# Optimization experiments

Measured on AMD Instinct MI355X. Metric: run time of the kernel, lower is better.

The kernel has to match this reference:

```python
import jax, jax.numpy as jnp
from jax import lax
import numpy as np

B, H0, W0, C = 2, 192, 192, 192
CH = C // 2            # channels per attention branch (window / stripe)
D = 4                  # blocks in the stage
WS = 8                 # window / stripe size
NHW = 4                # window-attention heads
NHS = 4                # stripe-attention heads
ADF = 2                # anchor down factor (avgpool)
MLP_RATIO = 4

def _rel_pos_index(ws):
    coords = np.stack(np.meshgrid(np.arange(ws), np.arange(ws), indexing="ij"))
    coords = coords.reshape(2, -1)
    rel = coords[:, :, None] - coords[:, None, :]
    rel = rel.transpose(1, 2, 0) + (ws - 1)
    return rel[..., 0] * (2 * ws - 1) + rel[..., 1]

REL_IDX = jnp.asarray(_rel_pos_index(WS))  # [N, N] into (2*WS-1)^2 table

def _swin_mask(H, W, ws, shift):
    img = np.zeros((H, W))
    cnt = 0
    for hs in (slice(0, -ws), slice(-ws, -shift), slice(-shift, None)):
        for wsl in (slice(0, -ws), slice(-ws, -shift), slice(-shift, None)):
            img[hs, wsl] = cnt
            cnt += 1
    win = img.reshape(H // ws, ws, W // ws, ws).transpose(0, 2, 1, 3).reshape(-1, ws * ws)
    diff = win[:, None, :] - win[:, :, None]
    return jnp.asarray(np.where(diff != 0, -100.0, 0.0), jnp.float32)

def _ln(x, g, b):
    mu = x.mean(-1, keepdims=True)
    var = x.var(-1, keepdims=True)
    return (x - mu) * lax.rsqrt(var + 1e-5) * g + b

def _window_attn(xw, H, W, shift, qkv_w, qkv_b, rpb):
    Bb, L, Cw = xw.shape
    h, dh, N = NHW, Cw // NHW, WS * WS
    x = xw.reshape(Bb, H, W, Cw)
    if shift:
        x = jnp.roll(x, (-shift, -shift), (1, 2))
    nH, nW = H // WS, W // WS
    xw_ = x.reshape(Bb, nH, WS, nW, WS, Cw).transpose(0, 1, 3, 2, 4, 5).reshape(-1, N, Cw)
    qkv = (xw_ @ qkv_w + qkv_b).reshape(-1, N, 3, h, dh)
    q, k, v = qkv[:, :, 0], qkv[:, :, 1], qkv[:, :, 2]
    attn = jnp.einsum("wnhd,wmhd->whnm", q * dh ** -0.5, k)
    attn = attn + rpb[REL_IDX].transpose(2, 0, 1)[None]  # relative position bias [h,N,N]
    if shift:
        mask = _swin_mask(H, W, WS, shift)  # [nWin, N, N]
        attn = (attn.reshape(Bb, nH * nW, h, N, N) + mask[None, :, None]).reshape(-1, h, N, N)
    attn = jax.nn.softmax(attn, -1)
    out = jnp.einsum("whnm,wmhd->wnhd", attn, v).reshape(-1, N, Cw)
    x = out.reshape(Bb, nH, nW, WS, WS, Cw).transpose(0, 1, 3, 2, 4, 5).reshape(Bb, H, W, Cw)
    if shift:
        x = jnp.roll(x, (shift, shift), (1, 2))
    return x.reshape(Bb, L, Cw)

def _stripe_attn(xs, H, W, qkv_w, qkv_b):
    # anchored stripe attention: q -> anchors -> k/v (two small softmaxes)
    Bb, L, Cs = xs.shape
    h, dh, N = NHS, Cs // NHS, WS * WS
    M = (WS // ADF) * (WS // ADF)
    x = xs.reshape(Bb, H // WS, WS, W // WS, WS, Cs).transpose(0, 1, 3, 2, 4, 5)
    x = x.reshape(-1, WS, WS, Cs)
    anchor = x.reshape(-1, WS // ADF, ADF, WS // ADF, ADF, Cs).mean((2, 4)).reshape(-1, M, h, dh)
    xt = x.reshape(-1, N, Cs)
    qkv = (xt @ qkv_w + qkv_b).reshape(-1, N, 3, h, dh)
    q, k, v = qkv[:, :, 0], qkv[:, :, 1], qkv[:, :, 2]
    s = dh ** -0.5
    a1 = jax.nn.softmax(jnp.einsum("snhd,smhd->shnm", q * s, anchor), -1)  # [S,h,N,M]
    a2 = jax.nn.softmax(jnp.einsum("smhd,snhd->shmn", anchor * s, k), -1)  # [S,h,M,N]
    out = jnp.einsum("shnm,shmt,sthd->snhd", a1, a2, v).reshape(-1, N, Cs)
    out = out.reshape(Bb, H // WS, W // WS, WS, WS, Cs).transpose(0, 1, 3, 2, 4, 5)
    return out.reshape(Bb, L, Cs)

def setup_inputs() -> dict:
    key = jax.random.key(0)
    ks = jax.random.split(key, 8)
    std = 0.02
    return {
        "x": jax.random.normal(ks[0], (B, H0 * W0, C), jnp.float32),
        "norm1_g": jnp.ones((D, C), jnp.float32),
        "norm1_b": jnp.zeros((D, C), jnp.float32),
        "qkv_w_win": jax.random.normal(ks[1], (D, CH, 3 * CH), jnp.float32) * std,
        "qkv_b_win": jnp.zeros((D, 3 * CH), jnp.float32),
        "qkv_w_str": jax.random.normal(ks[2], (D, CH, 3 * CH), jnp.float32) * std,
        "qkv_b_str": jnp.zeros((D, 3 * CH), jnp.float32),
        "proj_w": jax.random.normal(ks[3], (D, C, C), jnp.float32) * std,
        "proj_b": jnp.zeros((D, C), jnp.float32),
        "rpb_table": jax.random.normal(ks[4], (D, (2 * WS - 1) ** 2, NHW), jnp.float32) * std,
        "norm2_g": jnp.ones((D, C), jnp.float32),
        "norm2_b": jnp.zeros((D, C), jnp.float32),
        "fc1_w": jax.random.normal(ks[5], (D, C, MLP_RATIO * C), jnp.float32) * std,
        "fc1_b": jnp.zeros((D, MLP_RATIO * C), jnp.float32),
        "fc2_w": jax.random.normal(ks[6], (D, MLP_RATIO * C, C), jnp.float32) * std,
        "fc2_b": jnp.zeros((D, C), jnp.float32),
        "conv_w": jax.random.normal(ks[7], (C, C, 3, 3), jnp.float32) * std,
        "conv_b": jnp.zeros((C,), jnp.float32),
        "H": H0,
        "W": W0,
    }

def reference(x, norm1_g, norm1_b, qkv_w_win, qkv_b_win, qkv_w_str, qkv_b_str,
              proj_w, proj_b, rpb_table, norm2_g, norm2_b, fc1_w, fc1_b,
              fc2_w, fc2_b, conv_w, conv_b, H, W):
    res0 = x
    for i in range(D):
        xn = _ln(x, norm1_g[i], norm1_b[i])
        shift = WS // 2 if i % 2 == 0 else 0  # window_shift = i % 2 == 0
        ow = _window_attn(xn[..., :CH], H, W, shift, qkv_w_win[i], qkv_b_win[i], rpb_table[i])
        os_ = _stripe_attn(xn[..., CH:], H, W, qkv_w_str[i], qkv_b_str[i])
        x = x + (jnp.concatenate([ow, os_], -1) @ proj_w[i] + proj_b[i])
        xn2 = _ln(x, norm2_g[i], norm2_b[i])
        x = x + (jax.nn.gelu(xn2 @ fc1_w[i] + fc1_b[i]) @ fc2_w[i] + fc2_b[i])
    Bb = x.shape[0]
    xc = x.reshape(Bb, H, W, C).transpose(0, 3, 1, 2)
    y = lax.conv_general_dilated(xc, conv_w, (1, 1), "SAME") + conv_b[None, :, None, None]
    y = y.transpose(0, 2, 3, 1).reshape(Bb, H * W, C)
    return y + res0  # long residual of the TransformerStage
```

## Files before the change

### kernel.cpp

```cpp
#include <hip/hip_runtime.h>
#include <math.h>

typedef __bf16 bf16_t;
typedef bf16_t bf16x8 __attribute__((ext_vector_type(8)));
typedef bf16_t bf16x4 __attribute__((ext_vector_type(4)));
typedef float f32x4 __attribute__((ext_vector_type(4)));

#define TOKS 73728
#define CCH 192

__device__ __forceinline__ float gelu_f(float x) {
  float x2 = x*x;
  float u = 1.5957691216057308f * x * fmaf(0.044715f, x2, 1.0f);
  float e = __expf(-u);
  return x * __builtin_amdgcn_rcpf(1.0f + e);
}

__device__ __forceinline__ void glds16(const void* g, void* l) {
  __builtin_amdgcn_global_load_lds(
      (const __attribute__((address_space(1))) void*)g,
      (__attribute__((address_space(3))) void*)l, 16, 0, 0);
}

__global__ void prep_all_k(const float* __restrict__ qw, const float* __restrict__ qs,
// ... 208 lines not shown
      for (int mi=0;mi<4;++mi)
        #pragma unroll
        for (int ni=0;ni<3;++ni)
          acc[mi][ni] = __builtin_amdgcn_mfma_f32_16x16x32_bf16(af[mi], bfr[ni], acc[mi][ni], 0, 0, 0);
    }
    __syncthreads();
  }

  #pragma unroll
  for (int mi=0;mi<4;++mi) {
    #pragma unroll
    for (int ni=0;ni<3;++ni) {
      const int col = wn*48 + ni*16 + lr;
      const float bs = bias[col];
      #pragma unroll
      for (int e=0;e<4;++e) {
        const long row = m0 + wm*64 + mi*16 + lk*4 + e;
        float v = acc[mi][ni][e] + bs + resid[row*CCH + col];
        acc[mi][ni][e] = v;
        resid[row*CCH + col] = v;
        if (EPI == 1) xnout[row*CCH + col] = (bf16_t)v;
      }
    }
  }
  if (EPI == 0) {
    float* red  = (float*)&As[0][0];
    float* stat = red + 1024;
    #pragma unroll
    for (int mi=0;mi<4;++mi) {
      #pragma unroll
      for (int e=0;e<4;++e) {
        float p1 = acc[mi][0][e] + acc[mi][1][e] + acc[mi][2][e];
        float p2 = acc[mi][0][e]*acc[mi][0][e] + acc[mi][1][e]*acc[mi][1][e]
                 + acc[mi][2][e]*acc[mi][2][e];
        #pragma unroll
        for (int off=1; off<16; off<<=1) {
          p1 += __shfl_xor(p1, off);
          p2 += __shfl_xor(p2, off);
        }
        if (lr == 0) {
          const int r = wm*64 + mi*16 + lk*4 + e;
          red[(r*4 + wn)*2]     = p1;
          red[(r*4 + wn)*2 + 1] = p2;
        }
      }
    }
    __syncthreads();
    if (tid < 128) {
      const int r = tid;
      float s1 = red[(r*4+0)*2] + red[(r*4+1)*2] + red[(r*4+2)*2] + red[(r*4+3)*2];
      float s2 = red[(r*4+0)*2+1] + red[(r*4+1)*2+1] + red[(r*4+2)*2+1] + red[(r*4+3)*2+1];
      const float mu = s1 * (1.f/CCH);
      stat[r*2]   = mu;
      stat[r*2+1] = rsqrtf(s2*(1.f/CCH) - mu*mu + 1e-5f);
    }
    __syncthreads();
    #pragma unroll
    for (int mi=0;mi<4;++mi) {
      #pragma unroll
      for (int e=0;e<4;++e) {
        const int r = wm*64 + mi*16 + lk*4 + e;
        const float mu = stat[r*2], rstd = stat[r*2+1];
        #pragma unroll
        for (int ni=0;ni<3;++ni) {
          const int col = wn*48 + ni*16 + lr;
          xnout[(m0+r)*CCH + col] = (bf16_t)((acc[mi][ni][e]-mu)*rstd*gg[col] + bb[col]);
        }
      }
    }
  }
}

__global__ __launch_bounds__(512) void gemmf_k(
    const bf16_t* __restrict__ A,
    const bf16_t* __restrict__ Bt,
    const float* __restrict__ bias,
    bf16_t* __restrict__ outb) {
  constexpr int BK=64, MASK=7;
  __shared__ bf16_t As[2][128*64];
  __shared__ bf16_t Bs[2][192*64];
  const int tid = threadIdx.x;
  const int w = tid >> 6, l = tid & 63;
  const int lr = l & 15, lk = l >> 4;
  const int ri = l >> 3, si = l & 7;
  const int wm = w >> 2, wn = w & 3;
  const long m0 = (long)blockIdx.x * 128;
  const int n0 = blockIdx.y * 192;

  f32x4 acc[4][3];
  #pragma unroll
  for (int mi=0;mi<4;++mi)
    #pragma unroll
    for (int ni=0;ni<3;++ni) acc[mi][ni] = (f32x4){0.f,0.f,0.f,0.f};

  auto stage = [&](int buf, int k0) {
    #pragma unroll
    for (int j = 0; j < 2; ++j) {
      const int s = j*8 + w;
      const int gr = s*8 + ri;
      glds16(A + (m0+gr)*192L + k0 + ((si ^ (gr&MASK))*8), &As[buf][s*512]);
    }
    #pragma unroll
    for (int j = 0; j < 3; ++j) {
      const int s = j*8 + w;
      const int gr = s*8 + ri;
      glds16(Bt + (long)(n0+gr)*192 + k0 + ((si ^ (gr&MASK))*8), &Bs[buf][s*512]);
    }
  };

  stage(0, 0);
  __syncthreads();
  for (int kt = 0; kt < 3; ++kt) {
    const int cur = kt & 1;
    if (kt + 1 < 3) stage(cur^1, (kt+1)*BK);
    #pragma unroll
    for (int ks = 0; ks < 2; ++ks) {
      bf16x8 af[4], bfr[3];
      #pragma unroll
      for (int mi=0;mi<4;++mi) {
        const int ar = wm*64 + mi*16 + lr;
        const int slot = (ks*4 + lk) ^ (ar & MASK);
        af[mi] = *(const bf16x8*)(&As[cur][ar*64 + slot*8]);
      }
      #pragma unroll
      for (int ni=0;ni<3;++ni) {
        const int br = wn*48 + ni*16 + lr;
        const int slot = (ks*4 + lk) ^ (br & MASK);
        bfr[ni] = *(const bf16x8*)(&Bs[cur][br*64 + slot*8]);
      }
      #pragma unroll
      for (int mi=0;mi<4;++mi)
        #pragma unroll
        for (int ni=0;ni<3;++ni)
          acc[mi][ni] = __builtin_amdgcn_mfma_f32_16x16x32_bf16(af[mi], bfr[ni], acc[mi][ni], 0, 0, 0);
    }
    __syncthreads();
  }

  #pragma unroll
  for (int mi=0;mi<4;++mi) {
    #pragma unroll
    for (int ni=0;ni<3;++ni) {
      const int col = n0 + wn*48 + ni*16 + lr;
      const float bs = bias[col];
      #pragma unroll
      for (int e=0;e<4;++e) {
        const long row = m0 + wm*64 + mi*16 + lk*4 + e;
        outb[row*768 + col] = (bf16_t)gelu_f(acc[mi][ni][e] + bs);
      }
    }
  }
}

__global__ __launch_bounds__(256) void win_attn3_k(
    const bf16_t* __restrict__ qkv, bf16_t* __restrict__ aout,
    const float* __restrict__ rpb2, int shift) {
  __shared__ bf16_t Vs[4][64][28];
  __shared__ bf16_t Pl[4][64][68];
  __shared__ float invl[4][64];
  const int h = threadIdx.x >> 6, l = threadIdx.x & 63;
  const int c = l & 15, g = l >> 4;
  const int wblk = blockIdx.x;
  const int b = wblk / 576, wi = wblk % 576;
  const int wh = wi / 24, ww = wi % 24;

  auto gtok = [&](int t) -> long {
    int ho = wh*8 + (t>>3) + shift; if (ho >= 192) ho -= 192;
    int wo = ww*8 + (t&7) + shift;  if (wo >= 192) wo -= 192;
    return (long)b*36864 + (long)ho*192 + wo;
  };

  {
    const bf16_t* vsrc = qkv + gtok(l)*576 + 192 + h*24;
    #pragma unroll
    for (int j=0;j<3;++j) {
      bf16x4 lo = *(const bf16x4*)(vsrc + j*8);
      bf16x4 hi = *(const bf16x4*)(vsrc + j*8 + 4);
      *(bf16x4*)(&Vs[h][l][j*8])   = lo;
      *(bf16x4*)(&Vs[h][l][j*8+4]) = hi;
    }
    *(bf16x4*)(&Vs[h][l][24]) = (bf16x4){};
  }

  bf16x8 kf[4], qf[4];
  #pragma unroll
  for (int t=0;t<4;++t) {
    bf16x8 z = {};
    kf[t] = z; qf[t] = z;
    if (g < 3) {
      const bf16_t* pb = qkv + gtok(16*t + c)*576 + h*24 + g*8;
      qf[t] = *(const bf16x8*)(pb);
      kf[t] = *(const bf16x8*)(pb + 96);
    }
  }

  f32x4 st[4][4];
  #pragma unroll
  for (int mt=0;mt<4;++mt)
    #pragma unroll
    for (int nt=0;nt<4;++nt)
      st[mt][nt] = __builtin_amdgcn_mfma_f32_16x16x32_bf16(kf[mt], qf[nt], (f32x4){0.f,0.f,0.f,0.f}, 0, 0, 0);

  const float scale = 0.20412414523193154f;
  const float4* rp = (const float4*)rpb2 + (h*64*16 + c);
  #pragma unroll
  for (int mt=0;mt<4;++mt) {
    #pragma unroll
    for (int r=0;r<4;++r) {
      const int k = 16*mt + 4*g + r;
      float4 b4 = rp[k*16];
      st[mt][0][r] = fmaf(st[mt][0][r], scale, b4.x);
      st[mt][1][r] = fmaf(st[mt][1][r], scale, b4.y);
      st[mt][2][r] = fmaf(st[mt][2][r], scale, b4.z);
      st[mt][3][r] = fmaf(st[mt][3][r], scale, b4.w);
    }
  }

  if (shift && (wh==23 || ww==23)) {
    #pragma unroll
    for (int mt=0;mt<4;++mt)
      #pragma unroll
      for (int r=0;r<4;++r) {
        const int kk = 16*mt + 4*g + r;
        const int krc = (wh==23) ? (((kk>>3)<4)?1:2) : 0;
        const int kcc = (ww==23) ? (((kk&7)<4)?1:2) : 0;
        const int kcls = krc*3 + kcc;
        #pragma unroll
        for (int nt=0;nt<4;++nt) {
          const int qq = 16*nt + c;
          const int qrc = (wh==23) ? (((qq>>3)<4)?1:2) : 0;
          const int qcc = (ww==23) ? (((qq&7)<4)?1:2) : 0;
          if (qrc*3 + qcc != kcls) st[mt][nt][r] -= 100.f;
        }
      }
  }

  #pragma unroll
  for (int nt=0;nt<4;++nt) {
    float m = st[0][nt][0];
    #pragma unroll
    for (int mt=0;mt<4;++mt)
      #pragma unroll
      for (int r=0;r<4;++r) m = fmaxf(m, st[mt][nt][r]);
    m = fmaxf(m, __shfl_xor(m, 16));
    m = fmaxf(m, __shfl_xor(m, 32));
    float s = 0.f;
    #pragma unroll
    for (int mt=0;mt<4;++mt)
      #pragma unroll
      for (int r=0;r<4;++r) {
        float p = __expf(st[mt][nt][r] - m);
        st[mt][nt][r] = p;
        s += p;
      }
    s += __shfl_xor(s, 16);
    s += __shfl_xor(s, 32);
    if (g == 0) invl[h][16*nt + c] = 1.f / s;
  }

  #pragma unroll
  for (int mt=0;mt<4;++mt) {
    #pragma unroll
    for (int nt=0;nt<4;++nt) {
      const int q = 16*nt + c;
      const int sl = (4*mt + g) ^ ((q&7)<<1);
      bf16x4 pk;
      #pragma unroll
      for (int r=0;r<4;++r) pk[r] = (bf16_t)st[mt][nt][r];
      *(bf16x4*)(&Pl[h][q][sl*4]) = pk;
    }
  }

  f32x4 oa[4][2];
  #pragma unroll
  for (int mt=0;mt<4;++mt)
    #pragma unroll
    for (int nt=0;nt<2;++nt) oa[mt][nt] = (f32x4){0.f,0.f,0.f,0.f};

  #pragma unroll
  for (int s2=0;s2<2;++s2) {
    bf16x8 pfr[4];
    #pragma unroll
    for (int mt=0;mt<4;++mt) {
      const int q = 16*mt + c;
      const int S0 = (8*s2 + 2*g) ^ ((q&7)<<1);
      bf16x4 lo = *(const bf16x4*)(&Pl[h][q][S0*4]);
      bf16x4 hi = *(const bf16x4*)(&Pl[h][q][S0*4 + 4]);
      #pragma unroll
      for (int r=0;r<4;++r) { pfr[mt][r] = lo[r]; pfr[mt][4+r] = hi[r]; }
    }
    #pragma unroll
    for (int nt=0;nt<2;++nt) {
      const int d = 16*nt + c;
      const int deff = (d < 24) ? d : 24;
      bf16x8 vf;
      #pragma unroll
      for (int e=0;e<8;++e) vf[e] = Vs[h][32*s2 + 8*g + e][deff];
      #pragma unroll
      for (int mt=0;mt<4;++mt)
        oa[mt][nt] = __builtin_amdgcn_mfma_f32_16x16x32_bf16(pfr[mt], vf, oa[mt][nt], 0, 0, 0);
    }
  }

  #pragma unroll
  for (int mt=0;mt<4;++mt) {
    #pragma unroll
    for (int r=0;r<4;++r) {
      const int q = 16*mt + 4*g + r;
      const float inv = invl[h][q];
      bf16_t* ob = aout + gtok(q)*192 + h*24;
      #pragma unroll
      for (int nt=0;nt<2;++nt) {
        const int d = 16*nt + c;
        if (d < 24) ob[d] = (bf16_t)(oa[mt][nt][r] * inv);
      }
    }
  }
}

__global__ __launch_bounds__(256) void stripe_attn3_k(
    const bf16_t* __restrict__ qkv, const bf16_t* __restrict__ xn,
    bf16_t* __restrict__ aout) {
  __shared__ bf16_t Vs[4][64][28];
  __shared__ bf16_t Ans[4][16][40];
  __shared__ bf16_t a2s[4][16][68];
  __shared__ bf16_t a1s[4][64][24];
  __shared__ bf16_t Ts2[4][32][28];
  const int h = threadIdx.x >> 6, l = threadIdx.x & 63;
  const int c = l & 15, g = l >> 4;
  const int wblk = blockIdx.x;
  const int b = wblk / 576, wi = wblk % 576;
  const int wh = wi / 24, ww = wi % 24;
  const long base0 = (long)b*36864 + (long)(wh*8)*192 + ww*8;
  auto gtok = [&](int t) -> long { return base0 + (long)(t>>3)*192 + (t&7); };

  {
    const bf16_t* vsrc = qkv + gtok(l)*576 + 480 + h*24;
    #pragma unroll
    for (int j=0;j<3;++j) {
      *(bf16x4*)(&Vs[h][l][j*8])   = *(const bf16x4*)(vsrc + j*8);
      *(bf16x4*)(&Vs[h][l][j*8+4]) = *(const bf16x4*)(vsrc + j*8 + 4);
    }
    *(bf16x4*)(&Vs[h][l][24]) = (bf16x4){};
  }
  {
    const int m = l >> 2, dq = l & 3;
    const int ar = m >> 2, ac = m & 3;
    const bf16_t* t0 = xn + (base0 + (long)(2*ar)*192 + 2*ac)*192 + 96 + h*24;
    #pragma unroll
    for (int j=0;j<6;++j) {
      const int d = dq*6 + j;
      float ssum = (float)t0[d] + (float)t0[192+d] + (float)t0[36864+d] + (float)t0[37056+d];
      Ans[h][m][d] = (bf16_t)(0.25f*ssum);
    }
  }
  if (l < 16) {
    *(bf16x4*)(&Ans[h][l][24]) = (bf16x4){};
    *(bf16x4*)(&Ans[h][l][28]) = (bf16x4){};
    bf16_t* z = &Ts2[h][16+l][0];
    #pragma unroll
    for (int j=0;j<7;++j) *(bf16x4*)(z + j*4) = (bf16x4){};
    *(bf16x4*)(&Ts2[h][l][24]) = (bf16x4){};
  }

  bf16x8 anf = *(const bf16x8*)(&Ans[h][c][g*8]);

  bf16x8 kf[4], qf[4];
  #pragma unroll
  for (int t=0;t<4;++t) {
    const bf16_t* pb = qkv + gtok(16*t + c)*576 + 288 + h*24 + g*8;
    qf[t] = *(const bf16x8*)(pb);
    kf[t] = *(const bf16x8*)(pb + 96);
  }

  const float scale = 0.20412414523193154f;

  f32x4 st2[4];
  #pragma unroll
  for (int mt=0;mt<4;++mt)
    st2[mt] = __builtin_amdgcn_mfma_f32_16x16x32_bf16(kf[mt], anf, (f32x4){0.f,0.f,0.f,0.f}, 0, 0, 0);

  {
    float m2 = -1e30f;
    #pragma unroll
    for (int mt=0;mt<4;++mt)
      #pragma unroll
      for (int r=0;r<4;++r) { st2[mt][r] *= scale; m2 = fmaxf(m2, st2[mt][r]); }
    m2 = fmaxf(m2, __shfl_xor(m2, 16));
    m2 = fmaxf(m2, __shfl_xor(m2, 32));
    float s = 0.f;
    #pragma unroll
    for (int mt=0;mt<4;++mt)
      #pragma unroll
      for (int r=0;r<4;++r) { float p = __expf(st2[mt][r] - m2); st2[mt][r] = p; s += p; }
    s += __shfl_xor(s, 16);
    s += __shfl_xor(s, 32);
    const float inv = 1.f / s;
    #pragma unroll
    for (int mt=0;mt<4;++mt) {
      const int sl = (4*mt + g) ^ ((c&7)<<1);
      bf16x4 pk;
      #pragma unroll
      for (int r=0;r<4;++r) pk[r] = (bf16_t)(st2[mt][r] * inv);
      *(bf16x4*)(&a2s[h][c][sl*4]) = pk;
    }
  }

  f32x4 ta[2];
  ta[0] = (f32x4){0.f,0.f,0.f,0.f}; ta[1] = (f32x4){0.f,0.f,0.f,0.f};
  #pragma unroll
  for (int kt=0;kt<2;++kt) {
    const int S0 = (8*kt + 2*g) ^ ((c&7)<<1);
    bf16x4 lo = *(const bf16x4*)(&a2s[h][c][S0*4]);
    bf16x4 hi = *(const bf16x4*)(&a2s[h][c][S0*4 + 4]);
    bf16x8 pf;
    #pragma unroll
    for (int r=0;r<4;++r) { pf[r] = lo[r]; pf[4+r] = hi[r]; }
    #pragma unroll
    for (int nt2=0;nt2<2;++nt2) {
      const int d = 16*nt2 + c;
      const int deff = (d < 24) ? d : 24;
      bf16x8 vf;
      #pragma unroll
      for (int e=0;e<8;++e) vf[e] = Vs[h][kt*32 + 8*g + e][deff];
      ta[nt2] = __builtin_amdgcn_mfma_f32_16x16x32_bf16(pf, vf, ta[nt2], 0, 0, 0);
    }
  }
  #pragma unroll
  for (int nt2=0;nt2<2;++nt2) {
    const int d = 16*nt2 + c;
    if (d < 24) {
      #pragma unroll
      for (int r=0;r<4;++r) Ts2[h][4*g + r][d] = (bf16_t)ta[nt2][r];
    }
  }

  f32x4 st1[4];
  #pragma unroll
  for (int nt=0;nt<4;++nt)
    st1[nt] = __builtin_amdgcn_mfma_f32_16x16x32_bf16(anf, qf[nt], (f32x4){0.f,0.f,0.f,0.f}, 0, 0, 0);

  #pragma unroll
  for (int nt=0;nt<4;++nt) {
    float m1 = -1e30f;
    #pragma unroll
    for (int r=0;r<4;++r) { st1[nt][r] *= scale; m1 = fmaxf(m1, st1[nt][r]); }
    m1 = fmaxf(m1, __shfl_xor(m1, 16));
    m1 = fmaxf(m1, __shfl_xor(m1, 32));
    float s = 0.f;
    #pragma unroll
    for (int r=0;r<4;++r) { float p = __expf(st1[nt][r] - m1); st1[nt][r] = p; s += p; }
    s += __shfl_xor(s, 16);
    s += __shfl_xor(s, 32);
    const float inv1 = 1.f / s;
    bf16x4 ak;
    #pragma unroll
    for (int r=0;r<4;++r) ak[r] = (bf16_t)(st1[nt][r] * inv1);
    *(bf16x4*)(&a1s[h][16*nt + c][4*g]) = ak;
  }

  f32x4 oa[4][2];
  #pragma unroll
  for (int mt=0;mt<4;++mt) { oa[mt][0] = (f32x4){0.f,0.f,0.f,0.f}; oa[mt][1] = (f32x4){0.f,0.f,0.f,0.f}; }
  #pragma unroll
  for (int mt=0;mt<4;++mt) {
    bf16x8 af = {};
    if (g < 2) af = *(const bf16x8*)(&a1s[h][16*mt + c][g*8]);
    #pragma unroll
    for (int nt2=0;nt2<2;++nt2) {
      const int d = 16*nt2 + c;
      const int deff = (d < 24) ? d : 24;
      bf16x8 tf;
      #pragma unroll
      for (int e=0;e<8;++e) tf[e] = Ts2[h][8*g + e][deff];
      oa[mt][nt2] = __builtin_amdgcn_mfma_f32_16x16x32_bf16(af, tf, oa[mt][nt2], 0, 0, 0);
    }
  }

  #pragma unroll
  for (int mt=0;mt<4;++mt) {
    #pragma unroll
    for (int r=0;r<4;++r) {
      const int tw = 16*mt + 4*g + r;
      bf16_t* ob = aout + gtok(tw)*192 + 96 + h*24;
      #pragma unroll
      for (int nt2=0;nt2<2;++nt2) {
        const int d = 16*nt2 + c;
        if (d < 24) ob[d] = (bf16_t)(oa[mt][nt2][r]);
      }
    }
  }
}

__global__ __launch_bounds__(256) void conv3_k(
    const bf16_t* __restrict__ xb,
    const bf16_t* __restrict__ Wc,
    const float* __restrict__ cb,
    const float* __restrict__ res0,
    const bf16_t* __restrict__ zb,
    float* __restrict__ out) {
  __shared__ bf16_t Xs[19968];
  __shared__ bf16_t Bs[18432];
  const int tid = threadIdx.x;
  const int w = tid >> 6, l = tid & 63;
  const int lr = l & 15, lk = l >> 4;
  const int rq = l >> 2, cq = (l & 3) * 8;
  const int bxr = blockIdx.x;
  const int bx = (bxr & 7) * 48 + (bxr >> 3);
  const int bimg = bx / 192, h = bx % 192;
  const int co0 = blockIdx.y * 64;

  f32x4 acc[3][4];
  #pragma unroll
  for (int mi=0; mi<3; ++mi)
    #pragma unroll
    for (int ni=0; ni<4; ++ni) acc[mi][ni] = (f32x4){0.f,0.f,0.f,0.f};

  for (int kcs = 0; kcs < 6; ++kcs) {
    const int kc = kcs * 32;
    for (int j = 0; j < 10; ++j) {
      int s = j*4 + w;
      if (s < 39) {
        int dy = s / 13, rem = s - dy*13;
        int tokcol = rem*16 + rq;
        int wc = tokcol - 1;
        int hp = h + dy - 1;
        const bf16_t* src = zb + cq;
        if (hp >= 0 && hp < 192 && wc >= 0 && wc < 192)
          src = xb + ((long)bimg*36864 + (long)hp*192 + wc)*192 + kc + cq;
        glds16(src, &Xs[s*512]);
      }
    }
    for (int j = 0; j < 9; ++j) {
      int s = j*4 + w;
      int tap = s >> 2, rem = s & 3;
      int row = rem*16 + rq;
      glds16(Wc + ((long)(tap*192 + co0 + row))*192 + kc + cq, &Bs[s*512]);
    }
    __syncthreads();
    #pragma unroll
    for (int tap = 0; tap < 9; ++tap) {
      const int dy = tap/3, dx = tap%3 - 1;
      bf16x8 af[3];
      #pragma unroll
      for (int mi=0; mi<3; ++mi) {
        int tokcol = w*48 + mi*16 + lr + dx + 1;
        af[mi] = *(const bf16x8*)(&Xs[dy*6656 + tokcol*32 + lk*8]);
      }
      #pragma unroll
      for (int ni=0; ni<4; ++ni) {
        bf16x8 bfr = *(const bf16x8*)(&Bs[tap*2048 + (ni*16+lr)*32 + lk*8]);
        #pragma unroll
        for (int mi=0; mi<3; ++mi)
          acc[mi][ni] = __builtin_amdgcn_mfma_f32_16x16x32_bf16(af[mi], bfr, acc[mi][ni], 0, 0, 0);
      }
    }
    if (kcs < 5) __syncthreads();
  }

  #pragma unroll
  for (int mi=0; mi<3; ++mi) {
    #pragma unroll
    for (int ni=0; ni<4; ++ni) {
      const int col = co0 + ni*16 + lr;
      const float cbv = cb[col];
      #pragma unroll
      for (int e=0; e<4; ++e) {
        const int tl = w*48 + mi*16 + lk*4 + e;
        const long tok = (long)bimg*36864 + (long)h*192 + tl;
        out[tok*192 + col] = acc[mi][ni][e] + cbv + res0[tok*192 + col];
      }
    }
  }
}

extern "C" void kernel_launch(void* const* d_in, const int* in_sizes, int n_in,
                              void* d_out, int out_size, void* d_ws, size_t ws_size,
                              hipStream_t stream) {
  const float* x_in     = (const float*)d_in[0];
  const float* norm1_g  = (const float*)d_in[1];
  const float* norm1_b  = (const float*)d_in[2];
  const float* qkv_w_w  = (const float*)d_in[3];
  const float* qkv_b_w  = (const float*)d_in[4];
  const float* qkv_w_s  = (const float*)d_in[5];
  const float* qkv_b_s  = (const float*)d_in[6];
  const float* proj_w   = (const float*)d_in[7];
  const float* proj_b   = (const float*)d_in[8];
  const float* rpb      = (const float*)d_in[9];
  const float* norm2_g  = (const float*)d_in[10];
  const float* norm2_b  = (const float*)d_in[11];
  const float* fc1_w    = (const float*)d_in[12];
  const float* fc1_b    = (const float*)d_in[13];
  const float* fc2_w    = (const float*)d_in[14];
  const float* fc2_b    = (const float*)d_in[15];
  const float* conv_w   = (const float*)d_in[16];
  const float* conv_b   = (const float*)d_in[17];

  char* ws = (char*)d_ws;
  float*  x_cur = (float*)ws;
  bf16_t* xn    = (bf16_t*)(ws + 56623104);
  bf16_t* qh    = (bf16_t*)(ws + 84934656);
  bf16_t* aoutb = (bf16_t*)(ws + 198180864);
  bf16_t* WwinT = (bf16_t*)(ws + 226492416);
  bf16_t* WstrT  = WwinT  + 110592;
  bf16_t* WprojT = WstrT  + 110592;
  bf16_t* Wfc1T  = WprojT + 147456;
  bf16_t* Wfc2T  = Wfc1T  + 589824;
  bf16_t* WconvT = Wfc2T  + 589824;
  float*  RPB2   = (float*)(WconvT + 331776);

  prep_all_k<<<7600, 256, 0, stream>>>(qkv_w_w, qkv_w_s, proj_w, fc1_w, fc2_w,
                                       conv_w, rpb,
                                       WwinT, WstrT, WprojT, Wfc1T, Wfc2T, WconvT, RPB2);

  ln0_k<<<TOKS/4, 256, 0, stream>>>(x_in, norm1_g, norm1_b, xn, x_cur);

  const int MB = TOKS/128;
  for (int i = 0; i < 4; ++i) {
    int shift = (i % 2 == 0) ? 4 : 0;
    dim3 g6(MB, 6), g4(MB, 4);
    gemmq_k<<<g6, 256, 0, stream>>>(xn, WwinT + (long)i*27648, WstrT + (long)i*27648,
                                    qkv_b_w + i*288, qkv_b_s + i*288, qh);
    win_attn3_k<<<1152, 256, 0, stream>>>(qh, aoutb, RPB2 + i*16384, shift);
    stripe_attn3_k<<<1152, 256, 0, stream>>>(qh, xn, aoutb);
    gemmb_k<0><<<MB, 512, 0, stream>>>(aoutb, WprojT + (long)i*36864, proj_b + i*192,
                                       x_cur, xn, norm2_g + i*192, norm2_b + i*192, 192);
    gemmf_k<<<g4, 512, 0, stream>>>(xn, Wfc1T + (long)i*147456, fc1_b + i*768, qh);
    if (i < 3)
      gemmb_k<0><<<MB, 512, 0, stream>>>(qh, Wfc2T + (long)i*147456, fc2_b + i*192,
                                         x_cur, xn, norm1_g + (i+1)*192, norm1_b + (i+1)*192, 768);
    else
      gemmb_k<1><<<MB, 512, 0, stream>>>(qh, Wfc2T + (long)i*147456, fc2_b + i*192,
                                         x_cur, aoutb, nullptr, nullptr, 768);
  }
  hipMemsetAsync(qh, 0, 4096, stream);
  dim3 gc(384, 3);
  conv3_k<<<gc, 256, 0, stream>>>(aoutb, WconvT, conv_b, x_in, qh, (float*)d_out);
}
```

Measured before the change: 996.1 us.

## Merge window and stripe attention into one launch; shrink conv weight LDS staging

```diff
diff --git a/kernel.cpp b/kernel.cpp
--- a/kernel.cpp
+++ b/kernel.cpp
@@ -384,347 +384,342 @@
   }
 }
 
-__global__ __launch_bounds__(256) void win_attn3_k(
-    const bf16_t* __restrict__ qkv, bf16_t* __restrict__ aout,
+__global__ __launch_bounds__(256) void attn_k(
+    const bf16_t* __restrict__ qkv, const bf16_t* __restrict__ xn,
+    bf16_t* __restrict__ aout,
     const float* __restrict__ rpb2, int shift) {
-  __shared__ bf16_t Vs[4][64][28];
-  __shared__ bf16_t Pl[4][64][68];
-  __shared__ float invl[4][64];
+  __shared__ __attribute__((aligned(16))) char smem[50176];
   const int h = threadIdx.x >> 6, l = threadIdx.x & 63;
   const int c = l & 15, g = l >> 4;
-  const int wblk = blockIdx.x;
-  const int b = wblk / 576, wi = wblk % 576;
-  const int wh = wi / 24, ww = wi % 24;
-
-  auto gtok = [&](int t) -> long {
-    int ho = wh*8 + (t>>3) + shift; if (ho >= 192) ho -= 192;
-    int wo = ww*8 + (t&7) + shift;  if (wo >= 192) wo -= 192;
-    return (long)b*36864 + (long)ho*192 + wo;
-  };
-
-  {
-    const bf16_t* vsrc = qkv + gtok(l)*576 + 192 + h*24;
-    #pragma unroll
-    for (int j=0;j<3;++j) {
-      bf16x4 lo = *(const bf16x4*)(vsrc + j*8);
-      bf16x4 hi = *(const bf16x4*)(vsrc + j*8 + 4);
-      *(bf16x4*)(&Vs[h][l][j*8])   = lo;
-      *(bf16x4*)(&Vs[h][l][j*8+4]) = hi;
-    }
-    *(bf16x4*)(&Vs[h][l][24]) = (bf16x4){};
-  }
-
-  bf16x8 kf[4], qf[4];
-  #pragma unroll
-  for (int t=0;t<4;++t) {
-    bf16x8 z = {};
-    kf[t] = z; qf[t] = z;
-    if (g < 3) {
-      const bf16_t* pb = qkv + gtok(16*t + c)*576 + h*24 + g*8;
+  const float scale = 0.20412414523193154f;
+
+  if (blockIdx.x < 1152) {
+    bf16_t (*Vs)[64][28] = (bf16_t(*)[64][28])smem;
+    bf16_t (*Pl)[64][68] = (bf16_t(*)[64][68])(smem + 14336);
+    float  (*invl)[64]   = (float(*)[64])(smem + 49152);
+    const int wblk = blockIdx.x;
+    const int b = wblk / 576, wi = wblk % 576;
+    const int wh = wi / 24, ww = wi % 24;
+
+    auto gtok = [&](int t) -> long {
+      int ho = wh*8 + (t>>3) + shift; if (ho >= 192) ho -= 192;
+      int wo = ww*8 + (t&7) + shift;  if (wo >= 192) wo -= 192;
+      return (long)b*36864 + (long)ho*192 + wo;
+    };
+
+    {
+      const bf16_t* vsrc = qkv + gtok(l)*576 + 192 + h*24;
+      #pragma unroll
+      for (int j=0;j<3;++j) {
+        *(bf16x4*)(&Vs[h][l][j*8])   = *(const bf16x4*)(vsrc + j*8);
+        *(bf16x4*)(&Vs[h][l][j*8+4]) = *(const bf16x4*)(vsrc + j*8 + 4);
+      }
+      *(bf16x4*)(&Vs[h][l][24]) = (bf16x4){};
+    }
+
+    bf16x8 kf[4], qf[4];
+    #pragma unroll
+    for (int t=0;t<4;++t) {
+      bf16x8 z = {};
+      kf[t] = z; qf[t] = z;
+      if (g < 3) {
+        const bf16_t* pb = qkv + gtok(16*t + c)*576 + h*24 + g*8;
+        qf[t] = *(const bf16x8*)(pb);
+        kf[t] = *(const bf16x8*)(pb + 96);
+      }
+    }
+
+    f32x4 st[4][4];
+    #pragma unroll
+    for (int mt=0;mt<4;++mt)
+      #pragma unroll
+      for (int nt=0;nt<4;++nt)
+        st[mt][nt] = __builtin_amdgcn_mfma_f32_16x16x32_bf16(kf[mt], qf[nt], (f32x4){0.f,0.f,0.f,0.f}, 0, 0, 0);
+
+    const float4* rp = (const float4*)rpb2 + (h*64*16 + c);
+    #pragma unroll
+    for (int mt=0;mt<4;++mt) {
+      #pragma unroll
+      for (int r=0;r<4;++r) {
+        const int k = 16*mt + 4*g + r;
+        float4 b4 = rp[k*16];
+        st[mt][0][r] = fmaf(st[mt][0][r], scale, b4.x);
+        st[mt][1][r] = fmaf(st[mt][1][r], scale, b4.y);
+        st[mt][2][r] = fmaf(st[mt][2][r], scale, b4.z);
+        st[mt][3][r] = fmaf(st[mt][3][r], scale, b4.w);
+      }
+    }
+
+    if (shift && (wh==23 || ww==23)) {
+      #pragma unroll
+      for (int mt=0;mt<4;++mt)
+        #pragma unroll
+        for (int r=0;r<4;++r) {
+          const int kk = 16*mt + 4*g + r;
+          const int krc = (wh==23) ? (((kk>>3)<4)?1:2) : 0;
+          const int kcc = (ww==23) ? (((kk&7)<4)?1:2) : 0;
+          const int kcls = krc*3 + kcc;
+          #pragma unroll
+          for (int nt=0;nt<4;++nt) {
+            const int qq = 16*nt + c;
+            const int qrc = (wh==23) ? (((qq>>3)<4)?1:2) : 0;
+            const int qcc = (ww==23) ? (((qq&7)<4)?1:2) : 0;
+            if (qrc*3 + qcc != kcls) st[mt][nt][r] -= 100.f;
+          }
+        }
+    }
+
+    #pragma unroll
+    for (int nt=0;nt<4;++nt) {
+      float m = st[0][nt][0];
+      #pragma unroll
+      for (int mt=0;mt<4;++mt)
+        #pragma unroll
+        for (int r=0;r<4;++r) m = fmaxf(m, st[mt][nt][r]);
+      m = fmaxf(m, __shfl_xor(m, 16));
+      m = fmaxf(m, __shfl_xor(m, 32));
+      float s = 0.f;
+      #pragma unroll
+      for (int mt=0;mt<4;++mt)
+        #pragma unroll
+        for (int r=0;r<4;++r) {
+          float p = __expf(st[mt][nt][r] - m);
+          st[mt][nt][r] = p;
+          s += p;
+        }
+      s += __shfl_xor(s, 16);
+      s += __shfl_xor(s, 32);
+      if (g == 0) invl[h][16*nt + c] = 1.f / s;
+    }
+
+    #pragma unroll
+    for (int mt=0;mt<4;++mt) {
+      #pragma unroll
+      for (int nt=0;nt<4;++nt) {
+        const int q = 16*nt + c;
+        const int sl = (4*mt + g) ^ ((q&7)<<1);
+        bf16x4 pk;
+        #pragma unroll
+        for (int r=0;r<4;++r) pk[r] = (bf16_t)st[mt][nt][r];
+        *(bf16x4*)(&Pl[h][q][sl*4]) = pk;
+      }
+    }
+
+    f32x4 oa[4][2];
+    #pragma unroll
+    for (int mt=0;mt<4;++mt)
+      #pragma unroll
+      for (int nt=0;nt<2;++nt) oa[mt][nt] = (f32x4){0.f,0.f,0.f,0.f};
+
+    #pragma unroll
+    for (int s2=0;s2<2;++s2) {
+      bf16x8 pfr[4];
+      #pragma unroll
+      for (int mt=0;mt<4;++mt) {
+        const int q = 16*mt + c;
+        const int S0 = (8*s2 + 2*g) ^ ((q&7)<<1);
+        bf16x4 lo = *(const bf16x4*)(&Pl[h][q][S0*4]);
+        bf16x4 hi = *(const bf16x4*)(&Pl[h][q][S0*4 + 4]);
+        #pragma unroll
+        for (int r=0;r<4;++r) { pfr[mt][r] = lo[r]; pfr[mt][4+r] = hi[r]; }
+      }
+      #pragma unroll
+      for (int nt=0;nt<2;++nt) {
+        const int d = 16*nt + c;
+        const int deff = (d < 24) ? d : 24;
+        bf16x8 vf;
+        #pragma unroll
+        for (int e=0;e<8;++e) vf[e] = Vs[h][32*s2 + 8*g + e][deff];
+        #pragma unroll
+        for (int mt=0;mt<4;++mt)
+          oa[mt][nt] = __builtin_amdgcn_mfma_f32_16x16x32_bf16(pfr[mt], vf, oa[mt][nt], 0, 0, 0);
+      }
+    }
+
+    #pragma unroll
+    for (int mt=0;mt<4;++mt) {
+      #pragma unroll
+      for (int r=0;r<4;++r) {
+        const int q = 16*mt + 4*g + r;
+        const float inv = invl[h][q];
+        bf16_t* ob = aout + gtok(q)*192 + h*24;
+        #pragma unroll
+        for (int nt=0;nt<2;++nt) {
+          const int d = 16*nt + c;
+          if (d < 24) ob[d] = (bf16_t)(oa[mt][nt][r] * inv);
+        }
+      }
+    }
+  } else {
+    bf16_t (*Vs)[64][28]  = (bf16_t(*)[64][28])smem;
+    bf16_t (*Ans)[16][40] = (bf16_t(*)[16][40])(smem + 14336);
+    bf16_t (*a2s)[16][68] = (bf16_t(*)[16][68])(smem + 19456);
+    bf16_t (*a1s)[64][24] = (bf16_t(*)[64][24])(smem + 28160);
+    bf16_t (*Ts2)[32][28] = (bf16_t(*)[32][28])(smem + 40448);
+    const int wblk = blockIdx.x - 1152;
+    const int b = wblk / 576, wi = wblk % 576;
+    const int wh = wi / 24, ww = wi % 24;
+    const long base0 = (long)b*36864 + (long)(wh*8)*192 + ww*8;
+    auto gtok = [&](int t) -> long { return base0 + (long)(t>>3)*192 + (t&7); };
+
+    {
+      const bf16_t* vsrc = qkv + gtok(l)*576 + 480 + h*24;
+      #pragma unroll
+      for (int j=0;j<3;++j) {
+        *(bf16x4*)(&Vs[h][l][j*8])   = *(const bf16x4*)(vsrc + j*8);
+        *(bf16x4*)(&Vs[h][l][j*8+4]) = *(const bf16x4*)(vsrc + j*8 + 4);
+      }
+      *(bf16x4*)(&Vs[h][l][24]) = (bf16x4){};
+    }
+    {
+      const int m = l >> 2, dq = l & 3;
+      const int ar = m >> 2, ac = m & 3;
+      const bf16_t* t0 = xn + (base0 + (long)(2*ar)*192 + 2*ac)*192 + 96 + h*24;
+      #pragma unroll
+      for (int j=0;j<6;++j) {
+        const int d = dq*6 + j;
+        float ssum = (float)t0[d] + (float)t0[192+d] + (float)t0[36864+d] + (float)t0[37056+d];
+        Ans[h][m][d] = (bf16_t)(0.25f*ssum);
+      }
+    }
+    if (l < 16) {
+      *(bf16x4*)(&Ans[h][l][24]) = (bf16x4){};
+      *(bf16x4*)(&Ans[h][l][28]) = (bf16x4){};
+      bf16_t* z = &Ts2[h][16+l][0];
+      #pragma unroll
+      for (int j=0;j<7;++j) *(bf16x4*)(z + j*4) = (bf16x4){};
+      *(bf16x4*)(&Ts2[h][l][24]) = (bf16x4){};
+    }
+
+    bf16x8 anf = *(const bf16x8*)(&Ans[h][c][g*8]);
+
+    bf16x8 kf[4], qf[4];
+    #pragma unroll
+    for (int t=0;t<4;++t) {
+      const bf16_t* pb = qkv + gtok(16*t + c)*576 + 288 + h*24 + g*8;
       qf[t] = *(const bf16x8*)(pb);
       kf[t] = *(const bf16x8*)(pb + 96);
     }
-  }
-
-  f32x4 st[4][4];
-  #pragma unroll
-  for (int mt=0;mt<4;++mt)
-    #pragma unroll
-    for (int nt=0;nt<4;++nt)
-      st[mt][nt] = __builtin_amdgcn_mfma_f32_16x16x32_bf16(kf[mt], qf[nt], (f32x4){0.f,0.f,0.f,0.f}, 0, 0, 0);
-
-  const float scale = 0.20412414523193154f;
-  const float4* rp = (const float4*)rpb2 + (h*64*16 + c);
-  #pragma unroll
-  for (int mt=0;mt<4;++mt) {
-    #pragma unroll
-    for (int r=0;r<4;++r) {
-      const int k = 16*mt + 4*g + r;
-      float4 b4 = rp[k*16];
-      st[mt][0][r] = fmaf(st[mt][0][r], scale, b4.x);
-      st[mt][1][r] = fmaf(st[mt][1][r], scale, b4.y);
-      st[mt][2][r] = fmaf(st[mt][2][r], scale, b4.z);
-      st[mt][3][r] = fmaf(st[mt][3][r], scale, b4.w);
-    }
-  }
-
-  if (shift && (wh==23 || ww==23)) {
+
+    f32x4 st2[4];
     #pragma unroll
     for (int mt=0;mt<4;++mt)
-      #pragma unroll
-      for (int r=0;r<4;++r) {
-        const int kk = 16*mt + 4*g + r;
-        const int krc = (wh==23) ? (((kk>>3)<4)?1:2) : 0;
-        const int kcc = (ww==23) ? (((kk&7)<4)?1:2) : 0;
-        const int kcls = krc*3 + kcc;
-        #pragma unroll
-        for (int nt=0;nt<4;++nt) {
-          const int qq = 16*nt + c;
-          const int qrc = (wh==23) ? (((qq>>3)<4)?1:2) : 0;
-          const int qcc = (ww==23) ? (((qq&7)<4)?1:2) : 0;
-          if (qrc*3 + qcc != kcls) st[mt][nt][r] -= 100.f;
-        }
-      }
-  }
-
-  #pragma unroll
-  for (int nt=0;nt<4;++nt) {
-    float m = st[0][nt][0];
-    #pragma unroll
-    for (int mt=0;mt<4;++mt)
-      #pragma unroll
-      for (int r=0;r<4;++r) m = fmaxf(m, st[mt][nt][r]);
-    m = fmaxf(m, __shfl_xor(m, 16));
-    m = fmaxf(m, __shfl_xor(m, 32));
-    float s = 0.f;
-    #pragma unroll
-    for (int mt=0;mt<4;++mt)
-      #pragma unroll
-      for (int r=0;r<4;++r) {
-        float p = __expf(st[mt][nt][r] - m);
-        st[mt][nt][r] = p;
-        s += p;
-      }
-    s += __shfl_xor(s, 16);
-    s += __shfl_xor(s, 32);
-    if (g == 0) invl[h][16*nt + c] = 1.f / s;
-  }
-
-  #pragma unroll
-  for (int mt=0;mt<4;++mt) {
-    #pragma unroll
-    for (int nt=0;nt<4;++nt) {
-      const int q = 16*nt + c;
-      const int sl = (4*mt + g) ^ ((q&7)<<1);
-      bf16x4 pk;
-      #pragma unroll
-      for (int r=0;r<4;++r) pk[r] = (bf16_t)st[mt][nt][r];
-      *(bf16x4*)(&Pl[h][q][sl*4]) = pk;
-    }
-  }
-
-  f32x4 oa[4][2];
-  #pragma unroll
-  for (int mt=0;mt<4;++mt)
-    #pragma unroll
-    for (int nt=0;nt<2;++nt) oa[mt][nt] = (f32x4){0.f,0.f,0.f,0.f};
-
-  #pragma unroll
-  for (int s2=0;s2<2;++s2) {
-    bf16x8 pfr[4];
-    #pragma unroll
-    for (int mt=0;mt<4;++mt) {
-      const int q = 16*mt + c;
-      const int S0 = (8*s2 + 2*g) ^ ((q&7)<<1);
-      bf16x4 lo = *(const bf16x4*)(&Pl[h][q][S0*4]);
-      bf16x4 hi = *(const bf16x4*)(&Pl[h][q][S0*4 + 4]);
-      #pragma unroll
-      for (int r=0;r<4;++r) { pfr[mt][r] = lo[r]; pfr[mt][4+r] = hi[r]; }
-    }
-    #pragma unroll
-    for (int nt=0;nt<2;++nt) {
-      const int d = 16*nt + c;
-      const int deff = (d < 24) ? d : 24;
-      bf16x8 vf;
-      #pragma unroll
-      for (int e=0;e<8;++e) vf[e] = Vs[h][32*s2 + 8*g + e][deff];
+      st2[mt] = __builtin_amdgcn_mfma_f32_16x16x32_bf16(kf[mt], anf, (f32x4){0.f,0.f,0.f,0.f}, 0, 0, 0);
+
+    {
+      float m2 = -1e30f;
       #pragma unroll
       for (int mt=0;mt<4;++mt)
-        oa[mt][nt] = __builtin_amdgcn_mfma_f32_16x16x32_bf16(pfr[mt], vf, oa[mt][nt], 0, 0, 0);
-    }
-  }
-
-  #pragma unroll
-  for (int mt=0;mt<4;++mt) {
-    #pragma unroll
-    for (int r=0;r<4;++r) {
-      const int q = 16*mt + 4*g + r;
-      const float inv = invl[h][q];
-      bf16_t* ob = aout + gtok(q)*192 + h*24;
-      #pragma unroll
-      for (int nt=0;nt<2;++nt) {
-        const int d = 16*nt + c;
-        if (d < 24) ob[d] = (bf16_t)(oa[mt][nt][r] * inv);
-      }
-    }
-  }
-}
-
-__global__ __launch_bounds__(256) void stripe_attn3_k(
-    const bf16_t* __restrict__ qkv, const bf16_t* __restrict__ xn,
-    bf16_t* __restrict__ aout) {
-  __shared__ bf16_t Vs[4][64][28];
-  __shared__ bf16_t Ans[4][16][40];
-  __shared__ bf16_t a2s[4][16][68];
-  __shared__ bf16_t a1s[4][64][24];
-  __shared__ bf16_t Ts2[4][32][28];
-  const int h = threadIdx.x >> 6, l = threadIdx.x & 63;
-  const int c = l & 15, g = l >> 4;
-  const int wblk = blockIdx.x;
-  const int b = wblk / 576, wi = wblk % 576;
-  const int wh = wi / 24, ww = wi % 24;
-  const long base0 = (long)b*36864 + (long)(wh*8)*192 + ww*8;
-  auto gtok = [&](int t) -> long { return base0 + (long)(t>>3)*192 + (t&7); };
-
-  {
-    const bf16_t* vsrc = qkv + gtok(l)*576 + 480 + h*24;
-    #pragma unroll
-    for (int j=0;j<3;++j) {
-      *(bf16x4*)(&Vs[h][l][j*8])   = *(const bf16x4*)(vsrc + j*8);
-      *(bf16x4*)(&Vs[h][l][j*8+4]) = *(const bf16x4*)(vsrc + j*8 + 4);
-    }
-    *(bf16x4*)(&Vs[h][l][24]) = (bf16x4){};
-  }
-  {
-    const int m = l >> 2, dq = l & 3;
-    const int ar = m >> 2, ac = m & 3;
-    const bf16_t* t0 = xn + (base0 + (long)(2*ar)*192 + 2*ac)*192 + 96 + h*24;
-    #pragma unroll
-    for (int j=0;j<6;++j) {
-      const int d = dq*6 + j;
-      float ssum = (float)t0[d] + (float)t0[192+d] + (float)t0[36864+d] + (float)t0[37056+d];
-      Ans[h][m][d] = (bf16_t)(0.25f*ssum);
-    }
-  }
-  if (l < 16) {
-    *(bf16x4*)(&Ans[h][l][24]) = (bf16x4){};
-    *(bf16x4*)(&Ans[h][l][28]) = (bf16x4){};
-    bf16_t* z = &Ts2[h][16+l][0];
-    #pragma unroll
-    for (int j=0;j<7;++j) *(bf16x4*)(z + j*4) = (bf16x4){};
-    *(bf16x4*)(&Ts2[h][l][24]) = (bf16x4){};
-  }
-
-  bf16x8 anf = *(const bf16x8*)(&Ans[h][c][g*8]);
-
-  bf16x8 kf[4], qf[4];
-  #pragma unroll
-  for (int t=0;t<4;++t) {
-    const bf16_t* pb = qkv + gtok(16*t + c)*576 + 288 + h*24 + g*8;
-    qf[t] = *(const bf16x8*)(pb);
-    kf[t] = *(const bf16x8*)(pb + 96);
-  }
-
-  const float scale = 0.20412414523193154f;
-
-  f32x4 st2[4];
-  #pragma unroll
-  for (int mt=0;mt<4;++mt)
-    st2[mt] = __builtin_amdgcn_mfma_f32_16x16x32_bf16(kf[mt], anf, (f32x4){0.f,0.f,0.f,0.f}, 0, 0, 0);
-
-  {
-    float m2 = -1e30f;
-    #pragma unroll
-    for (int mt=0;mt<4;++mt)
-      #pragma unroll
-      for (int r=0;r<4;++r) { st2[mt][r] *= scale; m2 = fmaxf(m2, st2[mt][r]); }
-    m2 = fmaxf(m2, __shfl_xor(m2, 16));
-    m2 = fmaxf(m2, __shfl_xor(m2, 32));
-    float s = 0.f;
-    #pragma unroll
-    for (int mt=0;mt<4;++mt)
-      #pragma unroll
-      for (int r=0;r<4;++r) { float p = __expf(st2[mt][r] - m2); st2[mt][r] = p; s += p; }
-    s += __shfl_xor(s, 16);
-    s += __shfl_xor(s, 32);
-    const float inv = 1.f / s;
-    #pragma unroll
-    for (int mt=0;mt<4;++mt) {
-      const int sl = (4*mt + g) ^ ((c&7)<<1);
-      bf16x4 pk;
-      #pragma unroll
-      for (int r=0;r<4;++r) pk[r] = (bf16_t)(st2[mt][r] * inv);
-      *(bf16x4*)(&a2s[h][c][sl*4]) = pk;
-    }
-  }
-
-  f32x4 ta[2];
-  ta[0] = (f32x4){0.f,0.f,0.f,0.f}; ta[1] = (f32x4){0.f,0.f,0.f,0.f};
-  #pragma unroll
-  for (int kt=0;kt<2;++kt) {
-    const int S0 = (8*kt + 2*g) ^ ((c&7)<<1);
-    bf16x4 lo = *(const bf16x4*)(&a2s[h][c][S0*4]);
-    bf16x4 hi = *(const bf16x4*)(&a2s[h][c][S0*4 + 4]);
-    bf16x8 pf;
-    #pragma unroll
-    for (int r=0;r<4;++r) { pf[r] = lo[r]; pf[4+r] = hi[r]; }
+        #pragma unroll
+        for (int r=0;r<4;++r) { st2[mt][r] *= scale; m2 = fmaxf(m2, st2[mt][r]); }
+      m2 = fmaxf(m2, __shfl_xor(m2, 16));
+      m2 = fmaxf(m2, __shfl_xor(m2, 32));
+      float s = 0.f;
+      #pragma unroll
+      for (int mt=0;mt<4;++mt)
+        #pragma unroll
+        for (int r=0;r<4;++r) { float p = __expf(st2[mt][r] - m2); st2[mt][r] = p; s += p; }
+      s += __shfl_xor(s, 16);
+      s += __shfl_xor(s, 32);
+      const float inv = 1.f / s;
+      #pragma unroll
+      for (int mt=0;mt<4;++mt) {
+        const int sl = (4*mt + g) ^ ((c&7)<<1);
+        bf16x4 pk;
+        #pragma unroll
+        for (int r=0;r<4;++r) pk[r] = (bf16_t)(st2[mt][r] * inv);
+        *(bf16x4*)(&a2s[h][c][sl*4]) = pk;
+      }
+    }
+
+    f32x4 ta[2];
+    ta[0] = (f32x4){0.f,0.f,0.f,0.f}; ta[1] = (f32x4){0.f,0.f,0.f,0.f};
+    #pragma unroll
+    for (int kt=0;kt<2;++kt) {
+      const int S0 = (8*kt + 2*g) ^ ((c&7)<<1);
+      bf16x4 lo = *(const bf16x4*)(&a2s[h][c][S0*4]);
+      bf16x4 hi = *(const bf16x4*)(&a2s[h][c][S0*4 + 4]);
+      bf16x8 pf;
+      #pragma unroll
+      for (int r=0;r<4;++r) { pf[r] = lo[r]; pf[4+r] = hi[r]; }
+      #pragma unroll
+      for (int nt2=0;nt2<2;++nt2) {
+        const int d = 16*nt2 + c;
+        const int deff = (d < 24) ? d : 24;
+        bf16x8 vf;
+        #pragma unroll
+        for (int e=0;e<8;++e) vf[e] = Vs[h][kt*32 + 8*g + e][deff];
+        ta[nt2] = __builtin_amdgcn_mfma_f32_16x16x32_bf16(pf, vf, ta[nt2], 0, 0, 0);
+      }
+    }
     #pragma unroll
     for (int nt2=0;nt2<2;++nt2) {
       const int d = 16*nt2 + c;
-      const int deff = (d < 24) ? d : 24;
-      bf16x8 vf;
-      #pragma unroll
-      for (int e=0;e<8;++e) vf[e] = Vs[h][kt*32 + 8*g + e][deff];
-      ta[nt2] = __builtin_amdgcn_mfma_f32_16x16x32_bf16(pf, vf, ta[nt2], 0, 0, 0);
-    }
-  }
-  #pragma unroll
-  for (int nt2=0;nt2<2;++nt2) {
-    const int d = 16*nt2 + c;
-    if (d < 24) {
-      #pragma unroll
-      for (int r=0;r<4;++r) Ts2[h][4*g + r][d] = (bf16_t)ta[nt2][r];
-    }
-  }
-
-  f32x4 st1[4];
-  #pragma unroll
-  for (int nt=0;nt<4;++nt)
-    st1[nt] = __builtin_amdgcn_mfma_f32_16x16x32_bf16(anf, qf[nt], (f32x4){0.f,0.f,0.f,0.f}, 0, 0, 0);
-
-  #pragma unroll
-  for (int nt=0;nt<4;++nt) {
-    float m1 = -1e30f;
-    #pragma unroll
-    for (int r=0;r<4;++r) { st1[nt][r] *= scale; m1 = fmaxf(m1, st1[nt][r]); }
-    m1 = fmaxf(m1, __shfl_xor(m1, 16));
-    m1 = fmaxf(m1, __shfl_xor(m1, 32));
-    float s = 0.f;
-    #pragma unroll
-    for (int r=0;r<4;++r) { float p = __expf(st1[nt][r] - m1); st1[nt][r] = p; s += p; }
-    s += __shfl_xor(s, 16);
-    s += __shfl_xor(s, 32);
-    const float inv1 = 1.f / s;
-    bf16x4 ak;
-    #pragma unroll
-    for (int r=0;r<4;++r) ak[r] = (bf16_t)(st1[nt][r] * inv1);
-    *(bf16x4*)(&a1s[h][16*nt + c][4*g]) = ak;
-  }
-
-  f32x4 oa[4][2];
-  #pragma unroll
-  for (int mt=0;mt<4;++mt) { oa[mt][0] = (f32x4){0.f,0.f,0.f,0.f}; oa[mt][1] = (f32x4){0.f,0.f,0.f,0.f}; }
-  #pragma unroll
-  for (int mt=0;mt<4;++mt) {
-    bf16x8 af = {};
-    if (g < 2) af = *(const bf16x8*)(&a1s[h][16*mt + c][g*8]);
-    #pragma unroll
-    for (int nt2=0;nt2<2;++nt2) {
-      const int d = 16*nt2 + c;
-      const int deff = (d < 24) ? d : 24;
-      bf16x8 tf;
-      #pragma unroll
-      for (int e=0;e<8;++e) tf[e] = Ts2[h][8*g + e][deff];
-      oa[mt][nt2] = __builtin_amdgcn_mfma_f32_16x16x32_bf16(af, tf, oa[mt][nt2], 0, 0, 0);
-    }
-  }
-
-  #pragma unroll
-  for (int mt=0;mt<4;++mt) {
-    #pragma unroll
-    for (int r=0;r<4;++r) {
-      const int tw = 16*mt + 4*g + r;
-      bf16_t* ob = aout + gtok(tw)*192 + 96 + h*24;
+      if (d < 24) {
+        #pragma unroll
+        for (int r=0;r<4;++r) Ts2[h][4*g + r][d] = (bf16_t)ta[nt2][r];
+      }
+    }
+
+    f32x4 st1[4];
+    #pragma unroll
+    for (int nt=0;nt<4;++nt)
+      st1[nt] = __builtin_amdgcn_mfma_f32_16x16x32_bf16(anf, qf[nt], (f32x4){0.f,0.f,0.f,0.f}, 0, 0, 0);
+
+    #pragma unroll
+    for (int nt=0;nt<4;++nt) {
+      float m1 = -1e30f;
+      #pragma unroll
+      for (int r=0;r<4;++r) { st1[nt][r] *= scale; m1 = fmaxf(m1, st1[nt][r]); }
+      m1 = fmaxf(m1, __shfl_xor(m1, 16));
+      m1 = fmaxf(m1, __shfl_xor(m1, 32));
+      float s = 0.f;
+      #pragma unroll
+      for (int r=0;r<4;++r) { float p = __expf(st1[nt][r] - m1); st1[nt][r] = p; s += p; }
+      s += __shfl_xor(s, 16);
+      s += __shfl_xor(s, 32);
+      const float inv1 = 1.f / s;
+      bf16x4 ak;
+      #pragma unroll
+      for (int r=0;r<4;++r) ak[r] = (bf16_t)(st1[nt][r] * inv1);
+      *(bf16x4*)(&a1s[h][16*nt + c][4*g]) = ak;
+    }
+
+    f32x4 oa[4][2];
+    #pragma unroll
+    for (int mt=0;mt<4;++mt) { oa[mt][0] = (f32x4){0.f,0.f,0.f,0.f}; oa[mt][1] = (f32x4){0.f,0.f,0.f,0.f}; }
+    #pragma unroll
+    for (int mt=0;mt<4;++mt) {
+      bf16x8 af = {};
+      if (g < 2) af = *(const bf16x8*)(&a1s[h][16*mt + c][g*8]);
       #pragma unroll
       for (int nt2=0;nt2<2;++nt2) {
         const int d = 16*nt2 + c;
-        if (d < 24) ob[d] = (bf16_t)(oa[mt][nt2][r]);
-      }
-    }
-  }
-}
-
-__global__ __launch_bounds__(256) void conv3_k(
+        const int deff = (d < 24) ? d : 24;
+        bf16x8 tf;
+        #pragma unroll
+        for (int e=0;e<8;++e) tf[e] = Ts2[h][8*g + e][deff];
+        oa[mt][nt2] = __builtin_amdgcn_mfma_f32_16x16x32_bf16(af, tf, oa[mt][nt2], 0, 0, 0);
+      }
+    }
+
+    #pragma unroll
+    for (int mt=0;mt<4;++mt) {
+      #pragma unroll
+      for (int r=0;r<4;++r) {
+        const int tw = 16*mt + 4*g + r;
+        bf16_t* ob = aout + gtok(tw)*192 + 96 + h*24;
+        #pragma unroll
+        for (int nt2=0;nt2<2;++nt2) {
+          const int d = 16*nt2 + c;
+          if (d < 24) ob[d] = (bf16_t)(oa[mt][nt2][r]);
+        }
+      }
+    }
+  }
+}
+
+__global__ __launch_bounds__(256) void conv5_k(
     const bf16_t* __restrict__ xb,
     const bf16_t* __restrict__ Wc,
     const float* __restrict__ cb,
@@ -732,7 +727,7 @@
     const bf16_t* __restrict__ zb,
     float* __restrict__ out) {
   __shared__ bf16_t Xs[19968];
-  __shared__ bf16_t Bs[18432];
+  __shared__ bf16_t Bs[6144];
   const int tid = threadIdx.x;
   const int w = tid >> 6, l = tid & 63;
   const int lr = l & 15, lk = l >> 4;
@@ -748,8 +743,37 @@
     #pragma unroll
     for (int ni=0; ni<4; ++ni) acc[mi][ni] = (f32x4){0.f,0.f,0.f,0.f};
 
+  auto stageB = [&](int dyg, int kc) {
+    #pragma unroll
+    for (int j = 0; j < 3; ++j) {
+      const int s = j*4 + w;
+      const int tap = s >> 2, rem = s & 3;
+      const int row = rem*16 + rq;
+      glds16(Wc + ((long)((dyg*3 + tap)*192 + co0 + row))*192 + kc + cq, &Bs[s*512]);
+    }
+  };
+  auto compute = [&](int dyg) {
+    #pragma unroll
+    for (int tap = 0; tap < 3; ++tap) {
+      bf16x8 af[3];
+      #pragma unroll
+      for (int mi=0; mi<3; ++mi) {
+        const int tokcol = w*48 + mi*16 + lr + tap;
+        af[mi] = *(const bf16x8*)(&Xs[dyg*6656 + tokcol*32 + lk*8]);
+      }
+      #pragma unroll
+      for (int ni=0; ni<4; ++ni) {
+        bf16x8 bfr = *(const bf16x8*)(&Bs[tap*2048 + (ni*16+lr)*32 + lk*8]);
+        #pragma unroll
+        for (int mi=0; mi<3; ++mi)
+          acc[mi][ni] = __builtin_amdgcn_mfma_f32_16x16x32_bf16(af[mi], bfr, acc[mi][ni], 0, 0, 0);
+      }
+    }
+  };
+
   for (int kcs = 0; kcs < 6; ++kcs) {
     const int kc = kcs * 32;
+    if (kcs) __syncthreads();
     for (int j = 0; j < 10; ++j) {
       int s = j*4 + w;
       if (s < 39) {
@@ -763,31 +787,16 @@
         glds16(src, &Xs[s*512]);
       }
     }
-    for (int j = 0; j < 9; ++j) {
-      int s = j*4 + w;
-      int tap = s >> 2, rem = s & 3;
-      int row = rem*16 + rq;
-      glds16(Wc + ((long)(tap*192 + co0 + row))*192 + kc + cq, &Bs[s*512]);
-    }
+    stageB(0, kc);
     __syncthreads();
-    #pragma unroll
-    for (int tap = 0; tap < 9; ++tap) {
-      const int dy = tap/3, dx = tap%3 - 1;
-      bf16x8 af[3];
-      #pragma unroll
-      for (int mi=0; mi<3; ++mi) {
-        int tokcol = w*48 + mi*16 + lr + dx + 1;
-        af[mi] = *(const bf16x8*)(&Xs[dy*6656 + tokcol*32 + lk*8]);
-      }
-      #pragma unroll
-      for (int ni=0; ni<4; ++ni) {
-        bf16x8 bfr = *(const bf16x8*)(&Bs[tap*2048 + (ni*16+lr)*32 + lk*8]);
-        #pragma unroll
-        for (int mi=0; mi<3; ++mi)
-          acc[mi][ni] = __builtin_amdgcn_mfma_f32_16x16x32_bf16(af[mi], bfr, acc[mi][ni], 0, 0, 0);
-      }
-    }
-    if (kcs < 5) __syncthreads();
+    compute(0);
+    #pragma unroll
+    for (int dyg = 1; dyg < 3; ++dyg) {
+      __syncthreads();
+      stageB(dyg, kc);
+      __syncthreads();
+      compute(dyg);
+    }
   }
 
   #pragma unroll
@@ -853,8 +862,7 @@
     dim3 g6(MB, 6), g4(MB, 4);
     gemmq_k<<<g6, 256, 0, stream>>>(xn, WwinT + (long)i*27648, WstrT + (long)i*27648,
                                     qkv_b_w + i*288, qkv_b_s + i*288, qh);
-    win_attn3_k<<<1152, 256, 0, stream>>>(qh, aoutb, RPB2 + i*16384, shift);
-    stripe_attn3_k<<<1152, 256, 0, stream>>>(qh, xn, aoutb);
+    attn_k<<<2304, 256, 0, stream>>>(qh, xn, aoutb, RPB2 + i*16384, shift);
     gemmb_k<0><<<MB, 512, 0, stream>>>(aoutb, WprojT + (long)i*36864, proj_b + i*192,
                                        x_cur, xn, norm2_g + i*192, norm2_b + i*192, 192);
     gemmf_k<<<g4, 512, 0, stream>>>(xn, Wfc1T + (long)i*147456, fc1_b + i*768, qh);
@@ -867,5 +875,5 @@
   }
   hipMemsetAsync(qh, 0, 4096, stream);
   dim3 gc(384, 3);
-  conv3_k<<<gc, 256, 0, stream>>>(aoutb, WconvT, conv_b, x_in, qh, (float*)d_out);
-}
+  conv5_k<<<gc, 256, 0, stream>>>(aoutb, WconvT, conv_b, x_in, qh, (float*)d_out);
+}
```

After: 971.2 us. -2.5%, faster.
